# Kernel tuning notes

Measured on AMD Instinct MI355X. Metric: run time of the kernel, lower is better.

The kernel has to match this reference:

```python
import jax, jax.numpy as jnp
import numpy as np
from jax import lax

_CLIP_MIN = 1e-06
_CLIP_MAX = 1.0
_POS_ALPHA = 0.0005
NUM_CLASSES = 21
RADIUS = 3
HALF_D = RADIUS * RADIUS
POOL = 3
PAD = POOL // 2
IGNORE = 255
LAM = 0.5  # loss_weight_lambda, lambda_way=1


def _max_pool(x):
    # NCHW max pool, kernel=stride=3, padding=1
    return lax.reduce_window(x, -jnp.inf, lax.max,
                             (1, 1, POOL, POOL), (1, 1, POOL, POOL),
                             ((0, 0), (0, 0), (PAD, PAD), (PAD, PAD)))


def _get_pairs(x):
    # stack radius*radius shifted crops -> [N, C, r^2, nh, nw]
    h, w = x.shape[2], x.shape[3]
    nh, nw = h - RADIUS + 1, w - RADIUS + 1
    crops = [x[:, :, y:y + nh, xo:xo + nw] for y in range(RADIUS) for xo in range(RADIUS)]
    return jnp.stack(crops, axis=2)


def _log_det_by_cholesky(m):
    chol = jnp.linalg.cholesky(m)
    return 2.0 * jnp.sum(jnp.log(jnp.diagonal(chol, axis1=-2, axis2=-1) + 1e-08), axis=-1)


def _rmi_lower_bound(labels_4d, probs_4d):
    la = _max_pool(labels_4d)
    pr = _max_pool(probs_4d)
    n, c = la.shape[0], la.shape[1]
    la_v = _get_pairs(la).reshape(n, c, HALF_D, -1)   # [N,C,d,L]
    pr_v = _get_pairs(pr).reshape(n, c, HALF_D, -1)
    la_v = la_v - jnp.mean(la_v, axis=3, keepdims=True)
    pr_v = pr_v - jnp.mean(pr_v, axis=3, keepdims=True)
    la_cov = jnp.einsum('ncdl,ncel->ncde', la_v, la_v)
    pr_cov = jnp.einsum('ncdl,ncel->ncde', pr_v, pr_v)
    eye = jnp.eye(HALF_D, dtype=la_cov.dtype)
    pr_cov_inv = jnp.linalg.inv(pr_cov + eye * _POS_ALPHA)
    la_pr_cov = jnp.einsum('ncdl,ncel->ncde', la_v, pr_v)
    appro_var = la_cov - jnp.einsum('ncde,ncef,ncgf->ncdg', la_pr_cov, pr_cov_inv, la_pr_cov)
    rmi_now = 0.5 * _log_det_by_cholesky(appro_var + eye * _POS_ALPHA)  # [N,C]
    rmi_per_class = jnp.mean(rmi_now.reshape(-1, NUM_CLASSES), axis=0) / float(HALF_D)
    return jnp.sum(rmi_per_class)


def setup_inputs() -> dict:
    key = jax.random.key(0)
    k1, k2 = jax.random.split(key)
    score = jax.random.normal(k1, (4, NUM_CLASSES, 512, 512), dtype=jnp.float32)
    target = jax.random.randint(k2, (4, 512, 512), 0, NUM_CLASSES, dtype=jnp.int64)
    return {"score": score, "target": target}


def reference(score, target):
    # cross entropy with ignore_index=255, mean reduction
    logp = jax.nn.log_softmax(score, axis=1)                      # [N,C,H,W]
    valid_ce = (target != IGNORE)
    safe_t = jnp.where(valid_ce, target, 0)
    nll = -jnp.take_along_axis(logp, safe_t[:, None].astype(jnp.int32), axis=1)[:, 0]
    normal_loss = jnp.sum(jnp.where(valid_ce, nll, 0.0)) / jnp.sum(valid_ce.astype(jnp.float32))

    # valid one-hot labels and masked sigmoid probs
    mask = (target < NUM_CLASSES)                                 # [N,H,W]
    maskf = mask.astype(jnp.float32)
    onehot = jax.nn.one_hot((target * mask).astype(jnp.int32), NUM_CLASSES, dtype=jnp.float32)
    onehot = onehot * maskf[..., None]                            # [N,H,W,C]
    onehot = jnp.transpose(onehot, (0, 3, 1, 2))                  # [N,C,H,W]
    probs = jnp.clip(jax.nn.sigmoid(score) * maskf[:, None], _CLIP_MIN, _CLIP_MAX)

    rmi_loss = _rmi_lower_bound(onehot, probs)
    return LAM * normal_loss + rmi_loss * (1.0 - LAM)
```

## Files before the change

kernel.cpp:

```cpp
#include <hip/hip_runtime.h>
#include <cfloat>
#include <cmath>

#define DEVINL __device__ __forceinline__

constexpr int N_ = 4, C_ = 21, H_ = 512, W_ = 512;
constexpr int P_ = 171;
constexpr int Q_ = 169;
constexpr int NC_ = N_ * C_;
constexpr int HW_ = H_ * W_;
constexpr int PP_ = 29241;
constexpr int PROW_ = 192;
constexpr int PPAD_ = PROW_ * P_;
constexpr int NCOV_ = 189;
constexpr float EPS_ = 5e-4f;
constexpr int RC_ = 43;
constexpr int G_ = 43;

constexpr int NB_CE = N_ * HW_ / 4 / 256;
constexpr int NB_PL = (NC_ * P_ * G_ + 255) / 256;

typedef float f4_t __attribute__((ext_vector_type(4)));
typedef __attribute__((address_space(1))) const void gas_void;
typedef __attribute__((address_space(3))) void las_void;

DEVINL constexpr int tstart(int d) { return d * 9 - d * (d - 1) / 2; }

template <int CTRL>
DEVINL float dpp_add(float v) {
    int x = __builtin_amdgcn_update_dpp(0, __float_as_int(v), CTRL, 0xF, 0xF, false);
    return v + __int_as_float(x);
}

DEVINL float wave_sum63(float v) {
    v = dpp_add<0x111>(v);
    v = dpp_add<0x112>(v);
    v = dpp_add<0x114>(v);
    v = dpp_add<0x118>(v);
    v = dpp_add<0x142>(v);
    v = dpp_add<0x143>(v);
    return v;
}

__global__ __launch_bounds__(256) void k_bits(const int* __restrict__ target,
                                              unsigned* __restrict__ pack,
                                              float* __restrict__ cov) {
    int t = threadIdx.x;
    if (blockIdx.x == 0) {
        for (int k = t; k < NC_ * NCOV_ + 2; k += 256) cov[k] = 0.f;
    }
    int tid = blockIdx.x * 256 + t;
    if (tid >= N_ * PP_) return;
    int cell = tid % PP_;
    int n = tid / PP_;
    int j = cell % P_;
    int i = cell / P_;
    int hl = 3 * i - 1; if (hl < 0) hl = 0;
    int wl = 3 * j - 1; if (wl < 0) wl = 0;
    int hmax = 3 * i + 1, wmax = 3 * j + 1;
    const int* tb = target + (size_t)n * HW_;
    unsigned oh = 0, px = 0;
#pragma unroll
    for (int r = 0; r < 3; ++r) {
        int hh = hl + r;
        bool hv = hh <= hmax;
        const int* trow = tb + hh * W_;
#pragma unroll
        for (int dc = 0; dc < 3; ++dc) {
            int ww = wl + dc;
            int tv = trow[ww];
            if (hv && (ww <= wmax) && tv >= 0 && tv < C_) {
                oh |= 1u << tv;
                px |= 1u << (r * 3 + dc);
            }
        }
    }
    pack[tid] = oh | (px << 23);
}

template <int IDX>
DEVINL void do_cell(const float (&f)[3][16], unsigned pk, int c, float* prp, float* lap) {
    unsigned px = pk >> 23;
    float vm = -FLT_MAX;
#pragma unroll
    for (int r = 0; r < 3; ++r)
#pragma unroll
        for (int dc = 0; dc < 3; ++dc)
            vm = fmaxf(vm, ((px >> (r * 3 + dc)) & 1u) ? f[r][IDX + dc] : -FLT_MAX);
    float p = __builtin_amdgcn_rcpf(1.f + __expf(-vm));
    p = fminf(fmaxf(p, 1e-6f), 1.f);
    *prp = p;
    *lap = ((pk >> c) & 1u) ? 1.f : 0.f;
}

__global__ __launch_bounds__(256) void k_mix(const float* __restrict__ score,
                                             const int* __restrict__ target,
                                             const unsigned* __restrict__ pack,
                                             float* __restrict__ pr,
                                             float* __restrict__ la,
                                             float* __restrict__ cov) {
    __shared__ float lds[7 * 1024];
    __shared__ float rn[4], rc[4];
    int bid = blockIdx.x;
    int t = threadIdx.x;
    int wv = t >> 6, lane = t & 63;

    if (bid < NB_CE) {
        int n = bid >> 8;
        int bhw = (bid * 1024) & (HW_ - 1);
        const float* sp0 = score + (size_t)n * C_ * HW_ + bhw;
        int p0 = bid * 1024 + t * 4;
        int4 t4 = *(const int4*)(target + p0);

        float4 se = {0.f, 0.f, 0.f, 0.f};
        float4 stgt = {0.f, 0.f, 0.f, 0.f};
        for (int ph = 0; ph < 3; ++ph) {
#pragma unroll
            for (int u = 0; u < 7; ++u) {
                int c = ph * 7 + u;
                const float* g = sp0 + (size_t)c * HW_ + t * 4;
                float* l = &lds[u * 1024 + wv * 256];
                __builtin_amdgcn_global_load_lds((gas_void*)g, (las_void*)l,
                                                 16, 0, 0);
            }
            asm volatile("s_waitcnt vmcnt(0)" ::: "memory");
            __syncthreads();
#pragma unroll
            for (int u = 0; u < 7; ++u) {
                int c = ph * 7 + u;
                f4_t v = *(const f4_t*)&lds[u * 1024 + t * 4];
                se.x += __expf(v.x);
                se.y += __expf(v.y);
                se.z += __expf(v.z);
                se.w += __expf(v.w);
                if (t4.x == c) stgt.x = v.x;
                if (t4.y == c) stgt.y = v.y;
                if (t4.z == c) stgt.z = v.z;
                if (t4.w == c) stgt.w = v.w;
            }
            __syncthreads();
        }

        float nll = 0.f, cnt = 0.f;
        if (t4.x != 255) { nll += __logf(se.x) - stgt.x; cnt += 1.f; }
        if (t4.y != 255) { nll += __logf(se.y) - stgt.y; cnt += 1.f; }
        if (t4.z != 255) { nll += __logf(se.z) - stgt.z; cnt += 1.f; }
        if (t4.w != 255) { nll += __logf(se.w) - stgt.w; cnt += 1.f; }

        nll = wave_sum63(nll);
        cnt = wave_sum63(cnt);
        if (lane == 63) { rn[wv] = nll; rc[wv] = cnt; }
        __syncthreads();
        if (t == 0)
            atomicAdd(&cov[NC_ * NCOV_ + 0], rn[0] + rn[1] + rn[2] + rn[3]);
        if (t == 64)
            atomicAdd(&cov[NC_ * NCOV_ + 1], rc[0] + rc[1] + rc[2] + rc[3]);
    } else {
        int tid = (bid - NB_CE) * 256 + t;
        if (tid >= NC_ * P_ * G_) return;
        int g = tid % G_;
        int rest = tid / G_;
        int i = rest % P_;
        int ncidx = rest / P_;
        int n = ncidx / C_;
        int c = ncidx - n * C_;

        int hl = 3 * i - 1; if (hl < 0) hl = 0;
        int b = (g == 0) ? 0 : 12 * g - 4;
        int o3 = (b + 15 < W_) ? 12 : 8;

        const float* sb = score + (size_t)ncidx * HW_ + (size_t)hl * W_ + b;
        float f[3][16];
#pragma unroll
        for (int r = 0; r < 3; ++r) {
            const float* rp = sb + r * W_;
            float4 q0 = *(const float4*)(rp);
            float4 q1 = *(const float4*)(rp + 4);
            float4 q2 = *(const float4*)(rp + 8);
            float4 q3 = *(const float4*)(rp + o3);
            f[r][0] = q0.x;  f[r][1] = q0.y;  f[r][2] = q0.z;  f[r][3] = q0.w;
            f[r][4] = q1.x;  f[r][5] = q1.y;  f[r][6] = q1.z;  f[r][7] = q1.w;
            f[r][8] = q2.x;  f[r][9] = q2.y;  f[r][10] = q2.z; f[r][11] = q2.w;
            f[r][12] = q3.x; f[r][13] = q3.y; f[r][14] = q3.z; f[r][15] = q3.w;
        }

        const unsigned* pkp = pack + n * PP_ + i * P_ + 4 * g;
        size_t ob = (size_t)ncidx * PPAD_ + (size_t)i * PROW_ + 4 * g;
        if (g == 0) {
            do_cell<0>(f, pkp[0], c, pr + ob + 0, la + ob + 0);
            do_cell<2>(f, pkp[1], c, pr + ob + 1, la + ob + 1);
            do_cell<5>(f, pkp[2], c, pr + ob + 2, la + ob + 2);
            do_cell<8>(f, pkp[3], c, pr + ob + 3, la + ob + 3);
        } else {
            do_cell<3>(f, pkp[0], c, pr + ob + 0, la + ob + 0);
            do_cell<6>(f, pkp[1], c, pr + ob + 1, la + ob + 1);
            do_cell<9>(f, pkp[2], c, pr + ob + 2, la + ob + 2);
            if (4 * g + 3 < P_)
                do_cell<12>(f, pkp[3], c, pr + ob + 3, la + ob + 3);
        }
    }
}

template <int D0, int D1>
DEVINL void cov_tri(const float* __restrict__ X, float* __restrict__ cov,
                    int nc, int r0, int rend, int s2base,
                    int tid, float (*red)[27]) {
    constexpr int NS2 = ((9 - D0) * (10 - D0) - (9 - D1) * (10 - D1)) / 2;
    constexpr int RLO = D0 / 3;
    constexpr int KOFF = tstart(D0);
    float s2[NS2];
#pragma unroll
    for (int k = 0; k < NS2; ++k) s2[k] = 0.f;

    int nitems = (rend - r0) * G_;
    for (int idx = tid; idx < nitems; idx += 256) {
        int lr = idx / G_;
        int q = idx - lr * G_;
        int x0 = q * 4;
        const float* base = X + (size_t)(r0 + lr) * PROW_ + x0;
        float v[3][8];
#pragma unroll
        for (int r = RLO; r < 3; ++r) {
            float4 u0 = *(const float4*)(base + r * PROW_);
            float4 u1 = *(const float4*)(base + r * PROW_ + 4);
            v[r][0] = u0.x; v[r][1] = u0.y; v[r][2] = u0.z; v[r][3] = u0.w;
            v[r][4] = u1.x; v[r][5] = u1.y; v[r][6] = u1.z; v[r][7] = u1.w;
        }
#pragma unroll
        for (int p = 0; p < 4; ++p) {
            if (x0 + p < Q_) {
                int k = 0;
#pragma unroll
                for (int d = D0; d < D1; ++d)
#pragma unroll
                    for (int e = d; e < 9; ++e) {
                        s2[k] += v[d / 3][p + d % 3] * v[e / 3][p + e % 3];
                        ++k;
                    }
            }
        }
    }

    int lane = tid & 63, wv = tid >> 6;
#pragma unroll
    for (int k = 0; k < NS2; ++k) {
        float v2 = wave_sum63(s2[k]);
        if (lane == 63) red[wv][k] = v2;
    }
    __syncthreads();
    if (tid < NS2) {
        float v2 = red[0][tid] + red[1][tid] + red[2][tid] + red[3][tid];
        atomicAdd(&cov[nc * NCOV_ + s2base + KOFF + tid], v2);
    }
}

template <int RA>
DEVINL void cov_ab(const float* __restrict__ A, const float* __restrict__ B,
                   float* __restrict__ cov, int nc, int r0, int rend,
                   int tid, float (*red)[27]) {
    float sab[27];
#pragma unroll
    for (int k = 0; k < 27; ++k) sab[k] = 0.f;

    int nitems = (rend - r0) * G_;
    for (int idx = tid; idx < nitems; idx += 256) {
        int lr = idx / G_;
        int q = idx - lr * G_;
        int x0 = q * 4;
        size_t off = (size_t)(r0 + lr) * PROW_ + x0;
        float a[8];
        {
            float4 u0 = *(const float4*)(A + off + RA * PROW_);
            float4 u1 = *(const float4*)(A + off + RA * PROW_ + 4);
            a[0] = u0.x; a[1] = u0.y; a[2] = u0.z; a[3] = u0.w;
            a[4] = u1.x; a[5] = u1.y; a[6] = u1.z; a[7] = u1.w;
        }
#pragma unroll
        for (int r = 0; r < 3; ++r) {
            float b[8];
            {
                float4 w0 = *(const float4*)(B + off + r * PROW_);
                float4 w1 = *(const float4*)(B + off + r * PROW_ + 4);
                b[0] = w0.x; b[1] = w0.y; b[2] = w0.z; b[3] = w0.w;
                b[4] = w1.x; b[5] = w1.y; b[6] = w1.z; b[7] = w1.w;
            }
#pragma unroll
            for (int p = 0; p < 4; ++p) {
                if (x0 + p < Q_) {
#pragma unroll
                    for (int dm = 0; dm < 3; ++dm)
#pragma unroll
                        for (int e2 = 0; e2 < 3; ++e2)
                            sab[dm * 9 + r * 3 + e2] += a[p + dm] * b[p + e2];
                }
            }
        }
    }

    int lane = tid & 63, wv = tid >> 6;
#pragma unroll
    for (int k = 0; k < 27; ++k) {
        float v2 = wave_sum63(sab[k]);
        if (lane == 63) red[wv][k] = v2;
    }
    __syncthreads();
    if (tid < 27) {
        float v2 = red[0][tid] + red[1][tid] + red[2][tid] + red[3][tid];
        atomicAdd(&cov[nc * NCOV_ + 108 + RA * 27 + tid], v2);
    }
}

DEVINL void cov_s1(const float* __restrict__ LA, const float* __restrict__ PR,
                   float* __restrict__ cov, int nc, int r0, int rend,
                   int tid, float (*red)[27]) {
    float s1a[9], s1b[9];
#pragma unroll
    for (int k = 0; k < 9; ++k) { s1a[k] = 0.f; s1b[k] = 0.f; }

    int nitems = (rend - r0) * G_;
    for (int idx = tid; idx < nitems; idx += 256) {
        int lr = idx / G_;
        int q = idx - lr * G_;
        int x0 = q * 4;
        size_t off = (size_t)(r0 + lr) * PROW_ + x0;
#pragma unroll
        for (int r = 0; r < 3; ++r) {
            float va[8], vb[8];
            {
                float4 u0 = *(const float4*)(LA + off + r * PROW_);
                float4 u1 = *(const float4*)(LA + off + r * PROW_ + 4);
                va[0] = u0.x; va[1] = u0.y; va[2] = u0.z; va[3] = u0.w;
                va[4] = u1.x; va[5] = u1.y; va[6] = u1.z; va[7] = u1.w;
                float4 w0 = *(const float4*)(PR + off + r * PROW_);
                float4 w1 = *(const float4*)(PR + off + r * PROW_ + 4);
                vb[0] = w0.x; vb[1] = w0.y; vb[2] = w0.z; vb[3] = w0.w;
                vb[4] = w1.x; vb[5] = w1.y; vb[6] = w1.z; vb[7] = w1.w;
            }
#pragma unroll
            for (int p = 0; p < 4; ++p) {
                if (x0 + p < Q_) {
#pragma unroll
                    for (int dc = 0; dc < 3; ++dc) {
                        s1a[r * 3 + dc] += va[p + dc];
                        s1b[r * 3 + dc] += vb[p + dc];
                    }
                }
            }
        }
    }

    int lane = tid & 63, wv = tid >> 6;
#pragma unroll
    for (int k = 0; k < 9; ++k) {
        float v2 = wave_sum63(s1a[k]);
        if (lane == 63) red[wv][k] = v2;
    }
#pragma unroll
    for (int k = 0; k < 9; ++k) {
        float v2 = wave_sum63(s1b[k]);
        if (lane == 63) red[wv][9 + k] = v2;
    }
    __syncthreads();
    if (tid < 18) {
        float v2 = red[0][tid] + red[1][tid] + red[2][tid] + red[3][tid];
        atomicAdd(&cov[nc * NCOV_ + tid], v2);
    }
}

__global__ __launch_bounds__(256) void k_cov(const float* __restrict__ la,
                                             const float* __restrict__ pr,
                                             float* __restrict__ cov) {
    __shared__ float red[4][27];
    int nc = blockIdx.x;
    int chunk = blockIdx.y;
    int part = blockIdx.z;
    int r0 = chunk * RC_;
    int rend = r0 + RC_;
    if (rend > Q_) rend = Q_;
    int tid = threadIdx.x;
    const float* LA = la + (size_t)nc * PPAD_;
    const float* PR = pr + (size_t)nc * PPAD_;

    switch (part) {
        case 0: cov_tri<0, 3>(LA, cov, nc, r0, rend, 18, tid, red); break;
        case 1: cov_tri<3, 9>(LA, cov, nc, r0, rend, 18, tid, red); break;
        case 2: cov_tri<0, 3>(PR, cov, nc, r0, rend, 63, tid, red); break;
        case 3: cov_tri<3, 9>(PR, cov, nc, r0, rend, 63, tid, red); break;
        case 4: cov_ab<0>(LA, PR, cov, nc, r0, rend, tid, red); break;
        case 5: cov_ab<1>(LA, PR, cov, nc, r0, rend, tid, red); break;
        case 6: cov_ab<2>(LA, PR, cov, nc, r0, rend, tid, red); break;
        case 7: cov_s1(LA, PR, cov, nc, r0, rend, tid, red); break;
    }
}

__global__ __launch_bounds__(128) void k_final(const float* __restrict__ cov,
                                               float* __restrict__ out) {
    __shared__ float red[128];
    int t = threadIdx.x;
    float my = 0.f;
    if (t < NC_) {
        const float* S = cov + t * NCOV_;
        const float Lf = (float)(Q_ * Q_);
        float sA[9], sB[9];
#pragma unroll
        for (int d = 0; d < 9; ++d) { sA[d] = S[d]; sB[d] = S[9 + d]; }
        float laC[45], M[45], Cm[81];
        {
            int k = 0;
#pragma unroll
            for (int d = 0; d < 9; ++d)
#pragma unroll
                for (int e = d; e < 9; ++e) {
                    laC[k] = S[18 + k] - sA[d] * sA[e] / Lf;
                    M[k] = S[63 + k] - sB[d] * sB[e] / Lf + (d == e ? EPS_ : 0.f);
                    ++k;
                }
#pragma unroll
            for (int d = 0; d < 9; ++d)
#pragma unroll
                for (int e = 0; e < 9; ++e)
                    Cm[d * 9 + e] = S[108 + d * 9 + e] - sA[d] * sB[e] / Lf;
        }
#pragma unroll
        for (int j = 0; j < 9; ++j) {
            float s = M[tstart(j)];
#pragma unroll
            for (int k = 0; k < j; ++k) { float l = M[tstart(k) + (j - k)]; s -= l * l; }
            float dj = sqrtf(fmaxf(s, 1e-30f));
            M[tstart(j)] = dj;
            float inv = 1.f / dj;
#pragma unroll
            for (int i = j + 1; i < 9; ++i) {
                float s2 = M[tstart(j) + (i - j)];
#pragma unroll
                for (int k = 0; k < j; ++k)
                    s2 -= M[tstart(k) + (i - k)] * M[tstart(k) + (j - k)];
                M[tstart(j) + (i - j)] = s2 * inv;
            }
        }
#pragma unroll
        for (int p = 0; p < 9; ++p) {
#pragma unroll
            for (int i = 0; i < 9; ++i) {
                float s = Cm[p * 9 + i];
#pragma unroll
                for (int k = 0; k < i; ++k)
                    s -= M[tstart(k) + (i - k)] * Cm[p * 9 + k];
                Cm[p * 9 + i] = s / M[tstart(i)];
            }
        }
#pragma unroll
        for (int d = 0; d < 9; ++d)
#pragma unroll
            for (int e = d; e < 9; ++e) {
                float s = 0.f;
#pragma unroll
                for (int i = 0; i < 9; ++i) s += Cm[d * 9 + i] * Cm[e * 9 + i];
                laC[tstart(d) + (e - d)] -= s;
                if (d == e) laC[tstart(d)] += EPS_;
            }
        float rmi = 0.f;
#pragma unroll
        for (int j = 0; j < 9; ++j) {
            float s = laC[tstart(j)];
#pragma unroll
            for (int k = 0; k < j; ++k) { float l = laC[tstart(k) + (j - k)]; s -= l * l; }
            float dj = sqrtf(fmaxf(s, 0.f));
            laC[tstart(j)] = dj;
            float inv = 1.f / fmaxf(dj, 1e-30f);
#pragma unroll
            for (int i = j + 1; i < 9; ++i) {
                float s2 = laC[tstart(j) + (i - j)];
#pragma unroll
                for (int k = 0; k < j; ++k)
                    s2 -= laC[tstart(k) + (i - k)] * laC[tstart(k) + (j - k)];
                laC[tstart(j) + (i - j)] = s2 * inv;
            }
            rmi += __logf(dj + 1e-8f);
        }
        my = rmi;
    }
    red[t] = my;
    __syncthreads();
#pragma unroll
    for (int o = 64; o > 0; o >>= 1) {
        if (t < o) red[t] += red[t + o];
        __syncthreads();
    }
    if (t == 0) {
        float rmi_total = red[0] / 36.f;
        float ce = cov[NC_ * NCOV_ + 0] / cov[NC_ * NCOV_ + 1];
        out[0] = 0.5f * ce + 0.5f * rmi_total;
    }
}

extern "C" void kernel_launch(void* const* d_in, const int* in_sizes, int n_in,
                              void* d_out, int out_size, void* d_ws, size_t ws_size,
                              hipStream_t stream) {
    const float* score = (const float*)d_in[0];
    const int* target = (const int*)d_in[1];
    float* pr = (float*)d_ws;
    float* la = pr + (size_t)NC_ * PPAD_;
    float* cov = la + (size_t)NC_ * PPAD_;
    unsigned* pack = (unsigned*)(cov + NC_ * NCOV_ + 2);

    k_bits<<<dim3((N_ * PP_ + 255) / 256), dim3(256), 0, stream>>>(target, pack, cov);
    k_mix<<<dim3(NB_CE + NB_PL), dim3(256), 0, stream>>>(score, target, pack, pr, la, cov);
    k_cov<<<dim3(NC_, 4, 8), dim3(256), 0, stream>>>(la, pr, cov);
    k_final<<<dim3(1), dim3(128), 0, stream>>>(cov, (float*)d_out);
}
```

Before: 251.1 us.

## Fuse horizontal max-pool into cross-entropy pass and split vertical pooling kernel

The cross-entropy kernel now also computes a masked horizontal 3-wide max over the score rows it already stages in LDS, and writes a reduced intermediate (about one third the width) to workspace. A new pooling kernel then reads this intermediate to do the vertical max, sigmoid and label extraction. The goal is to avoid the second full read of the score tensor that the old pooling path made. In exchange it adds an extra kernel launch and an intermediate write and read, and the CE kernel now has smaller channel batches with more synchronisation.

Result: no change. 251.4 us (+0.1%).

```diff
diff --git a/kernel.cpp b/kernel.cpp
--- a/kernel.cpp
+++ b/kernel.cpp
@@ -16,8 +16,10 @@
 constexpr float EPS_ = 5e-4f;
 constexpr int RC_ = 43;
 constexpr int G_ = 43;
-
-constexpr int NB_CE = N_ * HW_ / 4 / 256;
+constexpr int HMROW_ = 172;
+constexpr int HMPL_ = 512 * HMROW_;
+
+constexpr int NB_CE = 1024;
 constexpr int NB_PL = (NC_ * P_ * G_ + 255) / 256;
 
 typedef float f4_t __attribute__((ext_vector_type(4)));
@@ -78,126 +80,134 @@
     pack[tid] = oh | (px << 23);
 }
 
-template <int IDX>
-DEVINL void do_cell(const float (&f)[3][16], unsigned pk, int c, float* prp, float* lap) {
-    unsigned px = pk >> 23;
-    float vm = -FLT_MAX;
-#pragma unroll
-    for (int r = 0; r < 3; ++r)
-#pragma unroll
-        for (int dc = 0; dc < 3; ++dc)
-            vm = fmaxf(vm, ((px >> (r * 3 + dc)) & 1u) ? f[r][IDX + dc] : -FLT_MAX);
-    float p = __builtin_amdgcn_rcpf(1.f + __expf(-vm));
-    p = fminf(fmaxf(p, 1e-6f), 1.f);
-    *prp = p;
-    *lap = ((pk >> c) & 1u) ? 1.f : 0.f;
-}
-
-__global__ __launch_bounds__(256) void k_mix(const float* __restrict__ score,
+__global__ __launch_bounds__(256) void k_ce2(const float* __restrict__ score,
                                              const int* __restrict__ target,
-                                             const unsigned* __restrict__ pack,
-                                             float* __restrict__ pr,
-                                             float* __restrict__ la,
+                                             float* __restrict__ hm,
                                              float* __restrict__ cov) {
-    __shared__ float lds[7 * 1024];
+    __shared__ float lds[4 * 1024];
+    __shared__ unsigned char lval[1024];
     __shared__ float rn[4], rc[4];
-    int bid = blockIdx.x;
+    int b = blockIdx.x;
     int t = threadIdx.x;
     int wv = t >> 6, lane = t & 63;
-
-    if (bid < NB_CE) {
-        int n = bid >> 8;
-        int bhw = (bid * 1024) & (HW_ - 1);
-        const float* sp0 = score + (size_t)n * C_ * HW_ + bhw;
-        int p0 = bid * 1024 + t * 4;
-        int4 t4 = *(const int4*)(target + p0);
-
-        float4 se = {0.f, 0.f, 0.f, 0.f};
-        float4 stgt = {0.f, 0.f, 0.f, 0.f};
-        for (int ph = 0; ph < 3; ++ph) {
-#pragma unroll
-            for (int u = 0; u < 7; ++u) {
-                int c = ph * 7 + u;
-                const float* g = sp0 + (size_t)c * HW_ + t * 4;
-                float* l = &lds[u * 1024 + wv * 256];
+    int n = b >> 8;
+    int brow = (b & 255) * 2;
+    int bhw = brow * W_;
+    const float* sp0 = score + (size_t)n * C_ * HW_ + bhw;
+
+    int4 t4 = *(const int4*)(target + (size_t)n * HW_ + bhw + t * 4);
+    unsigned vb = (unsigned)(t4.x >= 0 && t4.x < C_)
+                | ((unsigned)(t4.y >= 0 && t4.y < C_) << 8)
+                | ((unsigned)(t4.z >= 0 && t4.z < C_) << 16)
+                | ((unsigned)(t4.w >= 0 && t4.w < C_) << 24);
+    *(unsigned*)&lval[t * 4] = vb;
+
+    float4 se = {0.f, 0.f, 0.f, 0.f};
+    float4 stgt = {0.f, 0.f, 0.f, 0.f};
+    float* hmn = hm + (size_t)n * C_ * HMPL_ + (size_t)brow * HMROW_;
+
+    for (int ph = 0; ph < 6; ++ph) {
+        int c0 = ph * 4;
+        int np = (c0 + 4 <= C_) ? 4 : (C_ - c0);
+        if (wv < np) {
+            int c = c0 + wv;
+#pragma unroll
+            for (int k = 0; k < 4; ++k) {
+                const float* g = sp0 + (size_t)c * HW_ + k * 256 + lane * 4;
+                float* l = &lds[wv * 1024 + k * 256];
                 __builtin_amdgcn_global_load_lds((gas_void*)g, (las_void*)l,
                                                  16, 0, 0);
             }
-            asm volatile("s_waitcnt vmcnt(0)" ::: "memory");
-            __syncthreads();
-#pragma unroll
-            for (int u = 0; u < 7; ++u) {
-                int c = ph * 7 + u;
-                f4_t v = *(const f4_t*)&lds[u * 1024 + t * 4];
-                se.x += __expf(v.x);
-                se.y += __expf(v.y);
-                se.z += __expf(v.z);
-                se.w += __expf(v.w);
-                if (t4.x == c) stgt.x = v.x;
-                if (t4.y == c) stgt.y = v.y;
-                if (t4.z == c) stgt.z = v.z;
-                if (t4.w == c) stgt.w = v.w;
-            }
-            __syncthreads();
-        }
-
-        float nll = 0.f, cnt = 0.f;
-        if (t4.x != 255) { nll += __logf(se.x) - stgt.x; cnt += 1.f; }
-        if (t4.y != 255) { nll += __logf(se.y) - stgt.y; cnt += 1.f; }
-        if (t4.z != 255) { nll += __logf(se.z) - stgt.z; cnt += 1.f; }
-        if (t4.w != 255) { nll += __logf(se.w) - stgt.w; cnt += 1.f; }
-
-        nll = wave_sum63(nll);
-        cnt = wave_sum63(cnt);
-        if (lane == 63) { rn[wv] = nll; rc[wv] = cnt; }
+        }
+        asm volatile("s_waitcnt vmcnt(0)" ::: "memory");
         __syncthreads();
-        if (t == 0)
-            atomicAdd(&cov[NC_ * NCOV_ + 0], rn[0] + rn[1] + rn[2] + rn[3]);
-        if (t == 64)
-            atomicAdd(&cov[NC_ * NCOV_ + 1], rc[0] + rc[1] + rc[2] + rc[3]);
-    } else {
-        int tid = (bid - NB_CE) * 256 + t;
-        if (tid >= NC_ * P_ * G_) return;
-        int g = tid % G_;
-        int rest = tid / G_;
-        int i = rest % P_;
-        int ncidx = rest / P_;
-        int n = ncidx / C_;
-        int c = ncidx - n * C_;
-
-        int hl = 3 * i - 1; if (hl < 0) hl = 0;
-        int b = (g == 0) ? 0 : 12 * g - 4;
-        int o3 = (b + 15 < W_) ? 12 : 8;
-
-        const float* sb = score + (size_t)ncidx * HW_ + (size_t)hl * W_ + b;
-        float f[3][16];
-#pragma unroll
-        for (int r = 0; r < 3; ++r) {
-            const float* rp = sb + r * W_;
-            float4 q0 = *(const float4*)(rp);
-            float4 q1 = *(const float4*)(rp + 4);
-            float4 q2 = *(const float4*)(rp + 8);
-            float4 q3 = *(const float4*)(rp + o3);
-            f[r][0] = q0.x;  f[r][1] = q0.y;  f[r][2] = q0.z;  f[r][3] = q0.w;
-            f[r][4] = q1.x;  f[r][5] = q1.y;  f[r][6] = q1.z;  f[r][7] = q1.w;
-            f[r][8] = q2.x;  f[r][9] = q2.y;  f[r][10] = q2.z; f[r][11] = q2.w;
-            f[r][12] = q3.x; f[r][13] = q3.y; f[r][14] = q3.z; f[r][15] = q3.w;
-        }
-
-        const unsigned* pkp = pack + n * PP_ + i * P_ + 4 * g;
-        size_t ob = (size_t)ncidx * PPAD_ + (size_t)i * PROW_ + 4 * g;
-        if (g == 0) {
-            do_cell<0>(f, pkp[0], c, pr + ob + 0, la + ob + 0);
-            do_cell<2>(f, pkp[1], c, pr + ob + 1, la + ob + 1);
-            do_cell<5>(f, pkp[2], c, pr + ob + 2, la + ob + 2);
-            do_cell<8>(f, pkp[3], c, pr + ob + 3, la + ob + 3);
-        } else {
-            do_cell<3>(f, pkp[0], c, pr + ob + 0, la + ob + 0);
-            do_cell<6>(f, pkp[1], c, pr + ob + 1, la + ob + 1);
-            do_cell<9>(f, pkp[2], c, pr + ob + 2, la + ob + 2);
-            if (4 * g + 3 < P_)
-                do_cell<12>(f, pkp[3], c, pr + ob + 3, la + ob + 3);
-        }
+
+        for (int u = 0; u < np; ++u) {
+            int cc = c0 + u;
+            f4_t v = *(const f4_t*)&lds[u * 1024 + t * 4];
+            se.x += __expf(v.x);
+            se.y += __expf(v.y);
+            se.z += __expf(v.z);
+            se.w += __expf(v.w);
+            if (t4.x == cc) stgt.x = v.x;
+            if (t4.y == cc) stgt.y = v.y;
+            if (t4.z == cc) stgt.z = v.z;
+            if (t4.w == cc) stgt.w = v.w;
+        }
+
+        int nit = np * 342;
+        for (int it = t; it < nit; it += 256) {
+            int u = it / 342;
+            int rem = it - u * 342;
+            int r = rem / 171;
+            int j = rem - r * 171;
+            int wl = 3 * j - 1; if (wl < 0) wl = 0;
+            int wmax = 3 * j + 1;
+            const float* ls = &lds[u * 1024 + r * 512];
+            const unsigned char* lv = &lval[r * 512];
+            float m = -FLT_MAX;
+#pragma unroll
+            for (int dc = 0; dc < 3; ++dc) {
+                int ww = wl + dc;
+                if (ww <= wmax && lv[ww]) m = fmaxf(m, ls[ww]);
+            }
+            hmn[(size_t)(c0 + u) * HMPL_ + (size_t)r * HMROW_ + j] = m;
+        }
+        __syncthreads();
+    }
+
+    float nll = 0.f, cnt = 0.f;
+    if (t4.x != 255) { nll += __logf(se.x) - stgt.x; cnt += 1.f; }
+    if (t4.y != 255) { nll += __logf(se.y) - stgt.y; cnt += 1.f; }
+    if (t4.z != 255) { nll += __logf(se.z) - stgt.z; cnt += 1.f; }
+    if (t4.w != 255) { nll += __logf(se.w) - stgt.w; cnt += 1.f; }
+
+    nll = wave_sum63(nll);
+    cnt = wave_sum63(cnt);
+    if (lane == 63) { rn[wv] = nll; rc[wv] = cnt; }
+    __syncthreads();
+    if (t == 0)
+        atomicAdd(&cov[NC_ * NCOV_ + 0], rn[0] + rn[1] + rn[2] + rn[3]);
+    if (t == 64)
+        atomicAdd(&cov[NC_ * NCOV_ + 1], rc[0] + rc[1] + rc[2] + rc[3]);
+}
+
+__global__ __launch_bounds__(256) void k_pool2(const float* __restrict__ hm,
+                                               const unsigned* __restrict__ pack,
+                                               float* __restrict__ pr,
+                                               float* __restrict__ la) {
+    int tid = blockIdx.x * 256 + threadIdx.x;
+    if (tid >= NC_ * P_ * G_) return;
+    int g = tid % G_;
+    int rest = tid / G_;
+    int i = rest % P_;
+    int ncidx = rest / P_;
+    int n = ncidx / C_;
+    int c = ncidx - n * C_;
+
+    int hl = 3 * i - 1; if (hl < 0) hl = 0;
+    int nr = (i == 0) ? 2 : 3;
+    const float* hp = hm + (size_t)ncidx * HMPL_ + (size_t)hl * HMROW_ + 4 * g;
+    f4_t m = {-FLT_MAX, -FLT_MAX, -FLT_MAX, -FLT_MAX};
+    for (int rr = 0; rr < nr; ++rr) {
+        f4_t v = *(const f4_t*)(hp + (size_t)rr * HMROW_);
+        m.x = fmaxf(m.x, v.x);
+        m.y = fmaxf(m.y, v.y);
+        m.z = fmaxf(m.z, v.z);
+        m.w = fmaxf(m.w, v.w);
+    }
+    const unsigned* pkp = pack + n * PP_ + i * P_ + 4 * g;
+    size_t ob = (size_t)ncidx * PPAD_ + (size_t)i * PROW_ + 4 * g;
+
+    float p0 = fminf(fmaxf(__builtin_amdgcn_rcpf(1.f + __expf(-m.x)), 1e-6f), 1.f);
+    float p1 = fminf(fmaxf(__builtin_amdgcn_rcpf(1.f + __expf(-m.y)), 1e-6f), 1.f);
+    float p2 = fminf(fmaxf(__builtin_amdgcn_rcpf(1.f + __expf(-m.z)), 1e-6f), 1.f);
+    pr[ob + 0] = p0; la[ob + 0] = ((pkp[0] >> c) & 1u) ? 1.f : 0.f;
+    pr[ob + 1] = p1; la[ob + 1] = ((pkp[1] >> c) & 1u) ? 1.f : 0.f;
+    pr[ob + 2] = p2; la[ob + 2] = ((pkp[2] >> c) & 1u) ? 1.f : 0.f;
+    if (4 * g + 3 < P_) {
+        float p3 = fminf(fmaxf(__builtin_amdgcn_rcpf(1.f + __expf(-m.w)), 1e-6f), 1.f);
+        pr[ob + 3] = p3; la[ob + 3] = ((pkp[3] >> c) & 1u) ? 1.f : 0.f;
     }
 }
 
@@ -501,11 +511,13 @@
     const int* target = (const int*)d_in[1];
     float* pr = (float*)d_ws;
     float* la = pr + (size_t)NC_ * PPAD_;
-    float* cov = la + (size_t)NC_ * PPAD_;
+    float* hm = la + (size_t)NC_ * PPAD_;
+    float* cov = hm + (size_t)NC_ * HMPL_;
     unsigned* pack = (unsigned*)(cov + NC_ * NCOV_ + 2);
 
     k_bits<<<dim3((N_ * PP_ + 255) / 256), dim3(256), 0, stream>>>(target, pack, cov);
-    k_mix<<<dim3(NB_CE + NB_PL), dim3(256), 0, stream>>>(score, target, pack, pr, la, cov);
+    k_ce2<<<dim3(NB_CE), dim3(256), 0, stream>>>(score, target, hm, cov);
+    k_pool2<<<dim3(NB_PL), dim3(256), 0, stream>>>(hm, pack, pr, la);
     k_cov<<<dim3(NC_, 4, 8), dim3(256), 0, stream>>>(la, pr, cov);
     k_final<<<dim3(1), dim3(128), 0, stream>>>(cov, (float*)d_out);
 }
```
